# Performance work log

Hardware: AMD Instinct MI355X
Metric: run time of the kernel (lower is better)

The kernel has to match this reference:

```python
import jax, jax.numpy as jnp
from jax import lax
import numpy as np

B, T, F = 4, 2048, 128
DM, L, STRIDE, KF = 512, 4, 4, 2
N, DC, E = 16, 4, 2
DI = E * DM          # 1024 inner dim
R = (DM + 15) // 16  # 32 dt_rank
K = KF * STRIDE      # 8 front conv kernel
EPS = 1e-5

def _ln(x, w, b):
    m = x.mean(-1, keepdims=True)
    v = ((x - m) ** 2).mean(-1, keepdims=True)
    return (x - m) / jnp.sqrt(v + EPS) * w + b

def _causal_dwconv(x, w, b):
    # x: (B,Ts,DI), w: (DI,DC) depthwise causal conv
    xc = x.transpose(0, 2, 1)
    y = lax.conv_general_dilated(xc, w[:, None, :], (1,), [(DC - 1, 0)],
                                 feature_group_count=w.shape[0])
    return (y + b[None, :, None]).transpose(0, 2, 1)

def _selective_scan(dt, A, Bm, Cm, u):
    # dt,u: (B,Ts,DI); A: (DI,N); Bm,Cm: (B,Ts,N)
    dA = jnp.exp(dt[..., None] * A)                  # (B,Ts,DI,N)
    dBu = (dt * u)[..., None] * Bm[:, :, None, :]    # (B,Ts,DI,N)
    def step(h, inp):
        dA_t, dBu_t, C_t = inp
        h = dA_t * h + dBu_t
        y = jnp.einsum('bdn,bn->bd', h, C_t)
        return h, y
    h0 = jnp.zeros((u.shape[0], DI, N), u.dtype)
    _, ys = lax.scan(step, h0, (dA.transpose(1, 0, 2, 3),
                                dBu.transpose(1, 0, 2, 3),
                                Cm.transpose(1, 0, 2)))
    return ys.transpose(1, 0, 2)

def _mamba(x, in_w, cw, cb, xp_w, dtp_w, dtp_b, A_log, Dp, out_w):
    xz = jnp.einsum('btd,ed->bte', x, in_w)          # (B,Ts,2*DI)
    xi, z = jnp.split(xz, 2, axis=-1)
    xi = jax.nn.silu(_causal_dwconv(xi, cw, cb))
    x_dbl = jnp.einsum('btd,ed->bte', xi, xp_w)      # (B,Ts,R+2N)
    dt, Bm, Cm = jnp.split(x_dbl, [R, R + N], axis=-1)
    dt = jax.nn.softplus(jnp.einsum('btr,dr->btd', dt, dtp_w) + dtp_b)
    y = _selective_scan(dt, -jnp.exp(A_log), Bm, Cm, xi)
    y = (y + xi * Dp) * jax.nn.silu(z)
    return jnp.einsum('btd,od->bto', y, out_w)

def _forward(x, conv_w, conv_b, in_proj_w, conv1d_w, conv1d_b, x_proj_w,
             dt_proj_w, dt_proj_b, A_log, D_skip, ln_w, ln_b, out_proj_w,
             norm_w, norm_b):
    T_orig = x.shape[1]
    # causal strided front conv: pad (K-1,0), stride=STRIDE, then GELU
    h = lax.conv_general_dilated(x.transpose(0, 2, 1), conv_w, (STRIDE,),
                                 [(K - 1, 0)])
    h = jax.nn.gelu((h + conv_b[None, :, None]).transpose(0, 2, 1),
                    approximate=False)               # (B,T//STRIDE,DM)
    for l in range(L):
        hn = _ln(h, ln_w[l], ln_b[l])
        h = h + _mamba(hn, in_proj_w[l], conv1d_w[l], conv1d_b[l],
                       x_proj_w[l], dt_proj_w[l], dt_proj_b[l],
                       A_log[l], D_skip[l], out_proj_w[l])
    h = _ln(h, norm_w, norm_b)
    # repeat_interleave upsample back to original resolution
    return jnp.repeat(h, STRIDE, axis=1)[:, :T_orig, :]

def setup_inputs():
    key = jax.random.key(0)
    ks = jax.random.split(key, 8)
    g = lambda i, shape, s=0.02: jax.random.normal(ks[i], shape, jnp.float32) * s
    A_log = jnp.tile(jnp.log(jnp.arange(1, N + 1, dtype=jnp.float32)), (L, DI, 1))
    return dict(
        x=jax.random.normal(ks[0], (B, T, F), jnp.float32),
        conv_w=g(1, (DM, F, K)), conv_b=jnp.zeros((DM,), jnp.float32),
        in_proj_w=g(2, (L, 2 * DI, DM)),
        conv1d_w=g(3, (L, DI, DC), 0.2),
        conv1d_b=jnp.zeros((L, DI), jnp.float32),
        x_proj_w=g(4, (L, R + 2 * N, DI)),
        dt_proj_w=g(5, (L, DI, R), 0.1),
        dt_proj_b=jnp.full((L, DI), -2.0, jnp.float32),
        A_log=A_log,
        D_skip=jnp.ones((L, DI), jnp.float32),
        ln_w=jnp.ones((L, DM), jnp.float32),
        ln_b=jnp.zeros((L, DM), jnp.float32),
        out_proj_w=g(6, (L, DM, DI)),
        norm_w=jnp.ones((DM,), jnp.float32),
        norm_b=jnp.zeros((DM,), jnp.float32),
    )

def reference(x, conv_w, conv_b, in_proj_w, conv1d_w, conv1d_b, x_proj_w,
              dt_proj_w, dt_proj_b, A_log, D_skip, ln_w, ln_b, out_proj_w,
              norm_w, norm_b):
    return _forward(x, conv_w, conv_b, in_proj_w, conv1d_w, conv1d_b, x_proj_w,
                    dt_proj_w, dt_proj_b, A_log, D_skip, ln_w, ln_b, out_proj_w,
                    norm_w, norm_b)
```

## Files before the change

kernel.cpp:

```cpp
#include <hip/hip_runtime.h>
#include <hip/hip_bf16.h>

typedef unsigned short u16;
typedef u16 u16x8 __attribute__((ext_vector_type(8)));
typedef __bf16 bf16x8 __attribute__((ext_vector_type(8)));
typedef float f32x4 __attribute__((ext_vector_type(4)));

#define GLOAD16(gsrc, ldst) \
  __builtin_amdgcn_global_load_lds((const __attribute__((address_space(1))) void*)(gsrc), \
                                   (__attribute__((address_space(3))) void*)(ldst), 16, 0, 0)

__device__ __forceinline__ u16 f2bf(float f) {
  union { float f; unsigned u; } c; c.f = f;
  unsigned r = c.u + 0x7FFFu + ((c.u >> 16) & 1u);
  return (u16)(r >> 16);
}
__device__ __forceinline__ float bf2f(u16 v) {
  union { unsigned u; float f; } c; c.u = ((unsigned)v) << 16;
  return c.f;
}

__global__ __launch_bounds__(256) void cast_weights_k(
    const float* __restrict__ in_w, const float* __restrict__ xp_w,
    const float* __restrict__ out_w, const float* __restrict__ conv_w,
    const float* __restrict__ A_log, const float* __restrict__ c1w,
    u16* __restrict__ winb, u16* __restrict__ wxpb, u16* __restrict__ woutb,
    u16* __restrict__ wconvb, float* __restrict__ Apre, float* __restrict__ cwt) {
  int i = blockIdx.x * 256 + threadIdx.x;
  if (i < 1048576) {
    const float4 v = *(const float4*)(in_w + (size_t)i * 4);
    ushort2 lo = {f2bf(v.x), f2bf(v.y)}, hi = {f2bf(v.z), f2bf(v.w)};
    *(ushort2*)(winb + (size_t)i * 4) = lo;
    *(ushort2*)(winb + (size_t)i * 4 + 2) = hi;
    return;
  }
  i -= 1048576;
  if (i < 65536) {
    const float4 v = *(const float4*)(xp_w + (size_t)i * 4);
    ushort2 lo = {f2bf(v.x), f2bf(v.y)}, hi = {f2bf(v.z), f2bf(v.w)};
    *(ushort2*)(wxpb + (size_t)i * 4) = lo;
    *(ushort2*)(wxpb + (size_t)i * 4 + 2) = hi;
    return;
  }
  i -= 65536;
  if (i < 524288) {
    const float4 v = *(const float4*)(out_w + (size_t)i * 4);
    ushort2 lo = {f2bf(v.x), f2bf(v.y)}, hi = {f2bf(v.z), f2bf(v.w)};
    *(ushort2*)(woutb + (size_t)i * 4) = lo;
    *(ushort2*)(woutb + (size_t)i * 4 + 2) = hi;
    return;
  }
  i -= 524288;
  if (i < 131072) {
    const int m = i >> 8, r = (i & 255) * 4;
    const int kk = r >> 7, ff = r & 127;
    const float* src = conv_w + m * 1024 + kk;
    ushort2 lo = {f2bf(src[(ff + 0) * 8]), f2bf(src[(ff + 1) * 8])};
    ushort2 hi = {f2bf(src[(ff + 2) * 8]), f2bf(src[(ff + 3) * 8])};
    *(ushort2*)(wconvb + (size_t)i * 4) = lo;
    *(ushort2*)(wconvb + (size_t)i * 4 + 2) = hi;
    return;
  }
  i -= 131072;
  if (i < 16384) {
    const float4 v = *(const float4*)(A_log + (size_t)i * 4);
    float4 o;
    o.x = -__expf(v.x); o.y = -__expf(v.y); o.z = -__expf(v.z); o.w = -__expf(v.w);
    *(float4*)(Apre + (size_t)i * 4) = o;
    return;
  }
  i -= 16384;
  if (i < 4096) {
    const int og = i * 4, l = og >> 12, r = og & 4095;
    const int j = r >> 10, d0 = r & 1023;
    float4 o;
    o.x = c1w[l * 4096 + (d0 + 0) * 4 + j];
    o.y = c1w[l * 4096 + (d0 + 1) * 4 + j];
    o.z = c1w[l * 4096 + (d0 + 2) * 4 + j];
    o.w = c1w[l * 4096 + (d0 + 3) * 4 + j];
    *(float4*)(cwt + (size_t)i * 4) = o;
  }
}

__global__ __launch_bounds__(256) void im2col_k(const float* __restrict__ x,
                                                u16* __restrict__ xc) {
  const int i = blockIdx.x * 256 + threadIdx.x;
  const int col = (i & 255) * 4, tok = i >> 8;
  const int kk = col >> 7, ff = col & 127;
  const int b = tok >> 9, to = tok & 511;
  const int t = to * 4 + kk - 7;
  float4 v = {0.f, 0.f, 0.f, 0.f};
  if (t >= 0) v = *(const float4*)(x + ((size_t)b * 2048 + t) * 128 + ff);
  ushort2 lo = {f2bf(v.x), f2bf(v.y)}, hi = {f2bf(v.z), f2bf(v.w)};
  *(ushort2*)(xc + (size_t)i * 4) = lo;
  *(ushort2*)(xc + (size_t)i * 4 + 2) = hi;
}

template <int NW>
__global__ __launch_bounds__(NW * 64) void gemm2_k(
    const u16* __restrict__ A, int lda, const u16* __restrict__ Bw, int ldb,
    u16* __restrict__ C, int ldc, int Ks, size_t mn) {
  __shared__ __align__(16) char smem[NW * 32768];
  const int tid = threadIdx.x, lane = tid & 63, wid = tid >> 6;
  const int bm = blockIdx.x, bn = blockIdx.y;
  const int Kw = Ks / NW;
  const size_t koff = (size_t)blockIdx.z * Ks + (size_t)wid * Kw;
  char* base = smem + wid * 32768;
  const int srow = lane >> 2, sslot = lane & 3;
  const int nk = Kw >> 5;
  f32x4 acc[4][4] = {};

  auto stage = [&](int buf, int kt) {
#pragma unroll
    for (int c = 0; c < 8; ++c) {
      int lrow, gr, ldx; const u16* src;
      if (c < 4) { lrow = c * 16 + srow; gr = bm * 64 + lrow; src = A; ldx = lda; }
      else { lrow = (c - 4) * 16 + srow; gr = bn * 64 + lrow; src = Bw; ldx = ldb; }
      const int slot = sslot ^ ((lrow >> 1) & 3);
      GLOAD16(src + (size_t)gr * ldx + koff + kt * 32 + slot * 8,
              base + buf * 8192 + c * 1024);
    }
  };

  stage(0, 0);
  if (nk > 1) stage(1, 1);
  if (nk > 2) stage(2, 2);
  const int s = lane >> 4, r0 = lane & 15;
  for (int kt = 0; kt < nk; ++kt) {
    const int p = kt & 3;
    if (kt + 2 < nk)      asm volatile("s_waitcnt vmcnt(16)" ::: "memory");
    else if (kt + 1 < nk) asm volatile("s_waitcnt vmcnt(8)" ::: "memory");
    else                  asm volatile("s_waitcnt vmcnt(0)" ::: "memory");
    __builtin_amdgcn_sched_barrier(0);
    bf16x8 af[4], bfv[4];
#pragma unroll
    for (int i = 0; i < 4; ++i) {
      const int r = i * 16 + r0;
      af[i] = *(const bf16x8*)(base + p * 8192 + r * 64 + ((s ^ ((r >> 1) & 3)) << 4));
      bfv[i] = *(const bf16x8*)(base + p * 8192 + 4096 + r * 64 + ((s ^ ((r >> 1) & 3)) << 4));
    }
#pragma unroll
    for (int mi = 0; mi < 4; ++mi)
#pragma unroll
      for (int ni = 0; ni < 4; ++ni)
        acc[mi][ni] = __builtin_amdgcn_mfma_f32_16x16x32_bf16(af[mi], bfv[ni],
                                                              acc[mi][ni], 0, 0, 0);
    __builtin_amdgcn_sched_barrier(0);
    if (kt + 3 < nk) stage((kt + 3) & 3, kt + 3);
  }
  if constexpr (NW == 2) {
    if (wid == 1) {
      f32x4* dst = (f32x4*)(smem + 32768);
#pragma unroll
      for (int mi = 0; mi < 4; ++mi)
#pragma unroll
        for (int ni = 0; ni < 4; ++ni)
          dst[(mi * 4 + ni) * 64 + lane] = acc[mi][ni];
    }
    __syncthreads();
    if (wid == 1) return;
    const f32x4* src1 = (const f32x4*)(smem + 32768);
#pragma unroll
    for (int mi = 0; mi < 4; ++mi)
#pragma unroll
      for (int ni = 0; ni < 4; ++ni)
        acc[mi][ni] += src1[(mi * 4 + ni) * 64 + lane];
  }
  const int er0 = lane & 15, eg4 = lane >> 4;
  u16* Cz = C + (size_t)blockIdx.z * mn;
#pragma unroll
  for (int mi = 0; mi < 4; ++mi)
#pragma unroll
    for (int ni = 0; ni < 4; ++ni) {
      const int col = bn * 64 + ni * 16 + er0;
#pragma unroll
      for (int r = 0; r < 4; ++r) {
        const int row = bm * 64 + mi * 16 + eg4 * 4 + r;
        Cz[(size_t)row * ldc + col] = f2bf(acc[mi][ni][r]);
      }
    }
}

template <int MODE>
__global__ __launch_bounds__(256) void red_ln_k(
    const u16* __restrict__ P, float* __restrict__ h,
    const float* __restrict__ bias, const float* __restrict__ w,
    const float* __restrict__ bb, u16* __restrict__ o, float* __restrict__ oup) {
  const int row = blockIdx.x * 4 + (threadIdx.x >> 6);
  const int lane = threadIdx.x & 63;
  const size_t base = (size_t)row * 512 + lane * 8;
  float v[8];
  if constexpr (MODE == 0) {
#pragma unroll
    for (int j = 0; j < 8; ++j) v[j] = 0.f;
  } else {
    float4 a = *(const float4*)(h + base);
    float4 b4 = *(const float4*)(h + base + 4);
    v[0] = a.x; v[1] = a.y; v[2] = a.z; v[3] = a.w;
    v[4] = b4.x; v[5] = b4.y; v[6] = b4.z; v[7] = b4.w;
  }
#pragma unroll
  for (int s2 = 0; s2 < 4; ++s2) {
    const u16x8 pv = *(const u16x8*)(P + (size_t)s2 * 1048576 + base);
#pragma unroll
    for (int j = 0; j < 8; ++j) v[j] += bf2f(pv[j]);
  }
  if constexpr (MODE == 0) {
    const int col = lane * 8;
#pragma unroll
    for (int j = 0; j < 8; ++j) {
      const float t = v[j] + bias[col + j];
      v[j] = 0.5f * t * (1.f + erff(t * 0.70710678118f));
    }
  }
  if constexpr (MODE != 2) {
    float4 oa; oa.x = v[0]; oa.y = v[1]; oa.z = v[2]; oa.w = v[3];
    float4 ob; ob.x = v[4]; ob.y = v[5]; ob.z = v[6]; ob.w = v[7];
    *(float4*)(h + base) = oa;
    *(float4*)(h + base + 4) = ob;
  }
  float s = 0.f, sq = 0.f;
#pragma unroll
  for (int j = 0; j < 8; ++j) { s += v[j]; sq += v[j] * v[j]; }
  for (int off = 32; off; off >>= 1) { s += __shfl_xor(s, off); sq += __shfl_xor(sq, off); }
  const float m = s * (1.f / 512.f);
  const float rs = rsqrtf(sq * (1.f / 512.f) - m * m + 1e-5f);
  const float* wp = w + lane * 8; const float* bp = bb + lane * 8;
  float nv[8];
#pragma unroll
  for (int j = 0; j < 8; ++j) nv[j] = (v[j] - m) * rs * wp[j] + bp[j];
  if constexpr (MODE != 2) {
    uint4 uu;
    uu.x = (unsigned)f2bf(nv[0]) | ((unsigned)f2bf(nv[1]) << 16);
    uu.y = (unsigned)f2bf(nv[2]) | ((unsigned)f2bf(nv[3]) << 16);
    uu.z = (unsigned)f2bf(nv[4]) | ((unsigned)f2bf(nv[5]) << 16);
    uu.w = (unsigned)f2bf(nv[6]) | ((unsigned)f2bf(nv[7]) << 16);
    *(uint4*)(o + base) = uu;
  } else {
    const int bi = row >> 9, t0 = row & 511;
    float4 lo; lo.x = nv[0]; lo.y = nv[1]; lo.z = nv[2]; lo.w = nv[3];
    float4 hi; hi.x = nv[4]; hi.y = nv[5]; hi.z = nv[6]; hi.w = nv[7];
    float* obp = oup + ((size_t)bi * 2048 + (size_t)t0 * 4) * 512 + lane * 8;
#pragma unroll
    for (int q = 0; q < 4; ++q) {
      *(float4*)(obp + (size_t)q * 512) = lo;
      *(float4*)(obp + (size_t)q * 512 + 4) = hi;
    }
  }
}

__global__ __launch_bounds__(256) void redx_k(const u16* __restrict__ P,
                                              float* __restrict__ C) {
  const size_t i8 = ((size_t)blockIdx.x * 256 + threadIdx.x) * 8;
  if (i8 >= 131072) return;
  float v[8] = {};
#pragma unroll
  for (int s2 = 0; s2 < 4; ++s2) {
    const u16x8 pv = *(const u16x8*)(P + (size_t)s2 * 131072 + i8);
#pragma unroll
    for (int j = 0; j < 8; ++j) v[j] += bf2f(pv[j]);
  }
  float4 a; a.x = v[0]; a.y = v[1]; a.z = v[2]; a.w = v[3];
  float4 b; b.x = v[4]; b.y = v[5]; b.z = v[6]; b.w = v[7];
  *(float4*)(C + i8) = a;
  *(float4*)(C + i8 + 4) = b;
}

__global__ __launch_bounds__(256) void dtproj_k(const float* __restrict__ xdbl,
                                                const float* __restrict__ dtw,
                                                const float* __restrict__ dtbias,
                                                u16* __restrict__ dtbb) {
  __shared__ float xls[32 * 32];
  const int tid = threadIdx.x;
  const int dc = (blockIdx.x & 3) * 256;
  const int tg = (blockIdx.x >> 2) * 32;
  const int d = dc + tid;
  float4 w[8];
#pragma unroll
  for (int j = 0; j < 8; ++j) w[j] = *(const float4*)(dtw + (size_t)d * 32 + j * 4);
  for (int i = tid; i < 1024; i += 256) {
    const int t = i >> 5, r = i & 31;
    xls[i] = xdbl[(size_t)(tg + t) * 64 + r];
  }
  const float b = dtbias[d];
  __syncthreads();
  for (int t = 0; t < 32; ++t) {
    const float4* xr = (const float4*)&xls[t * 32];
    float acc = b;
#pragma unroll
    for (int j = 0; j < 8; ++j) {
      const float4 xv = xr[j];
      acc = fmaf(w[j].x, xv.x, acc); acc = fmaf(w[j].y, xv.y, acc);
      acc = fmaf(w[j].z, xv.z, acc); acc = fmaf(w[j].w, xv.w, acc);
    }
    dtbb[(size_t)(tg + t) * 1024 + d] =
        f2bf(fmaxf(acc, 0.f) + __logf(1.f + __expf(-fabsf(acc))));
  }
}

__global__ __launch_bounds__(256) void dwconv_k(const u16* __restrict__ xzb,
                                                const float* __restrict__ cwt,
                                                const float* __restrict__ cb,
                                                u16* __restrict__ xib) {
  const int i = blockIdx.x * 256 + threadIdx.x;
  const int d0 = (i & 127) * 8, tok = i >> 7, t = tok & 511;
  const u16* p = xzb + (size_t)tok * 2048 + d0;
  const float4 b0 = *(const float4*)(cb + d0);
  const float4 b1 = *(const float4*)(cb + d0 + 4);
  float acc[8] = {b0.x, b0.y, b0.z, b0.w, b1.x, b1.y, b1.z, b1.w};
#pragma unroll
  for (int j = 0; j < 4; ++j) {
    const int ts = t + j - 3;
    if (ts >= 0) {
      const u16x8 xv = *(const u16x8*)(p + (j - 3) * 2048);
      const float4 wa = *(const float4*)(cwt + j * 1024 + d0);
      const float4 wb = *(const float4*)(cwt + j * 1024 + d0 + 4);
      acc[0] = fmaf(bf2f(xv[0]), wa.x, acc[0]);
      acc[1] = fmaf(bf2f(xv[1]), wa.y, acc[1]);
      acc[2] = fmaf(bf2f(xv[2]), wa.z, acc[2]);
      acc[3] = fmaf(bf2f(xv[3]), wa.w, acc[3]);
      acc[4] = fmaf(bf2f(xv[4]), wb.x, acc[4]);
      acc[5] = fmaf(bf2f(xv[5]), wb.y, acc[5]);
      acc[6] = fmaf(bf2f(xv[6]), wb.z, acc[6]);
      acc[7] = fmaf(bf2f(xv[7]), wb.w, acc[7]);
    }
  }
  u16x8 o;
#pragma unroll
  for (int e = 0; e < 8; ++e)
    o[e] = f2bf(acc[e] / (1.f + __expf(-acc[e])));
  *(u16x8*)(xib + (size_t)i * 8) = o;
}

__global__ __launch_bounds__(256) void scan1_k(const u16* __restrict__ dtbb,
                                               const u16* __restrict__ xib,
                                               const float* __restrict__ xd,
                                               const float* __restrict__ Ap,
                                               float* __restrict__ hF,
                                               float* __restrict__ aP) {
  const int blk = blockIdx.x;
  const int d = (blk & 3) * 256 + threadIdx.x;
  const int c = (blk >> 2) & 31, b = blk >> 7;
  float A[16], h[16], ap[16];
#pragma unroll
  for (int n = 0; n < 16; ++n) { A[n] = Ap[d * 16 + n]; h[n] = 0.f; ap[n] = 1.f; }
  const int t0 = c * 16;
  for (int t = t0; t < t0 + 16; ++t) {
    const int tok = b * 512 + t;
    const float dtv = bf2f(dtbb[(size_t)tok * 1024 + d]);
    const float u = bf2f(xib[(size_t)tok * 1024 + d]);
    const float s = dtv * u;
    const float* Bp = xd + (size_t)tok * 64 + 32;
#pragma unroll
    for (int n = 0; n < 16; ++n) {
      const float dA = __expf(dtv * A[n]);
      h[n] = dA * h[n] + s * Bp[n];
      ap[n] *= dA;
    }
  }
#pragma unroll
  for (int n = 0; n < 16; ++n) {
    const size_t o = ((size_t)(b * 32 + c) * 16 + n) * 1024 + d;
    hF[o] = h[n]; aP[o] = ap[n];
  }
}

__global__ __launch_bounds__(256) void scan2_k(const float* __restrict__ hF,
                                               const float* __restrict__ aP,
                                               float* __restrict__ hI) {
  const int bi = blockIdx.x >> 6;
  const int n = (blockIdx.x >> 2) & 15;
  const int d = (blockIdx.x & 3) * 256 + threadIdx.x;
  float h = 0.f;
  for (int c = 0; c < 32; ++c) {
    const size_t o = ((size_t)((bi * 32 + c) * 16 + n)) * 1024 + d;
    hI[o] = h;
    h = fmaf(aP[o], h, hF[o]);
  }
}

__global__ __launch_bounds__(256) void scan3_k(const u16* __restrict__ dtbb,
                                               const u16* __restrict__ xib,
                                               const float* __restrict__ xd,
                                               const float* __restrict__ Ap,
                                               const float* __restrict__ hI,
                                               const u16* __restrict__ xzb,
                                               const float* __restrict__ Dp,
                                               u16* __restrict__ y2b) {
  const int blk = blockIdx.x;
  const int d = (blk & 3) * 256 + threadIdx.x;
  const int c = (blk >> 2) & 31, b = blk >> 7;
  float A[16], h[16];
#pragma unroll
  for (int n = 0; n < 16; ++n) {
    A[n] = Ap[d * 16 + n];
    h[n] = hI[((size_t)(b * 32 + c) * 16 + n) * 1024 + d];
  }
  const float Dd = Dp[d];
  const int t0 = c * 16;
  for (int t = t0; t < t0 + 16; ++t) {
    const int tok = b * 512 + t;
    const float dtv = bf2f(dtbb[(size_t)tok * 1024 + d]);
    const float u = bf2f(xib[(size_t)tok * 1024 + d]);
    const float s = dtv * u;
    const float* Bp = xd + (size_t)tok * 64 + 32;
    const float* Cp = xd + (size_t)tok * 64 + 48;
    float y = 0.f;
#pragma unroll
    for (int n = 0; n < 16; ++n) {
      const float dA = __expf(dtv * A[n]);
      h[n] = dA * h[n] + s * Bp[n];
      y = fmaf(h[n], Cp[n], y);
    }
    const float z = bf2f(xzb[(size_t)tok * 2048 + 1024 + d]);
    const float sz = z / (1.f + __expf(-z));
    y2b[(size_t)tok * 1024 + d] = f2bf((y + u * Dd) * sz);
  }
}

extern "C" void kernel_launch(void* const* d_in, const int* in_sizes, int n_in,
                              void* d_out, int out_size, void* d_ws, size_t ws_size,
                              hipStream_t stream) {
  const float* x      = (const float*)d_in[0];
  const float* conv_w = (const float*)d_in[1];
  const float* conv_b = (const float*)d_in[2];
  const float* in_w   = (const float*)d_in[3];
  const float* c1w    = (const float*)d_in[4];
  const float* c1b    = (const float*)d_in[5];
  const float* xp_w   = (const float*)d_in[6];
  const float* dt_w   = (const float*)d_in[7];
  const float* dt_b   = (const float*)d_in[8];
  const float* A_log  = (const float*)d_in[9];
  const float* D_skip = (const float*)d_in[10];
  const float* ln_w   = (const float*)d_in[11];
  const float* ln_b   = (const float*)d_in[12];
  const float* out_w  = (const float*)d_in[13];
  const float* norm_w = (const float*)d_in[14];
  const float* norm_b = (const float*)d_in[15];
  float* out = (float*)d_out;

  float* f = (float*)d_ws;
  float* h    = f; f += 1048576;
  float* xdbl = f; f += 131072;
  float* Apre = f; f += 65536;
  float* cwt  = f; f += 16384;
  float* hF   = f; f += 2097152;
  float* aP   = f; f += 2097152;
  float* hI   = f; f += 2097152;
  u16* ub = (u16*)f;
  u16* hnb    = ub; ub += 1048576;
  u16* xzb    = ub; ub += 4194304;
  u16* xib    = ub; ub += 2097152;
  u16* dtbb   = ub; ub += 2097152;
  u16* y2b    = ub; ub += 2097152;
  u16* xcolb  = ub; ub += 2097152;
  u16* pp     = ub; ub += 4194304;
  u16* ppB    = ub; ub += 524288;
  u16* winb   = ub; ub += 4194304;
  u16* wxpb   = ub; ub += 262144;
  u16* woutb  = ub; ub += 2097152;
  u16* wconvb = ub; ub += 524288;

  cast_weights_k<<<6993, 256, 0, stream>>>(in_w, xp_w, out_w, conv_w, A_log, c1w,
                                           winb, wxpb, woutb, wconvb, Apre, cwt);
  im2col_k<<<2048, 256, 0, stream>>>(x, xcolb);
  gemm2_k<2><<<dim3(32, 8, 4), 128, 0, stream>>>(xcolb, 1024, wconvb, 1024,
                                                 pp, 512, 256, (size_t)1048576);
  red_ln_k<0><<<512, 256, 0, stream>>>(pp, h, conv_b, ln_w, ln_b, hnb, nullptr);
  for (int l = 0; l < 4; ++l) {
    gemm2_k<2><<<dim3(32, 32, 1), 128, 0, stream>>>(hnb, 512, winb + l * 1048576,
                                                    512, xzb, 2048, 512, 0);
    dwconv_k<<<1024, 256, 0, stream>>>(xzb, cwt + l * 4096, c1b + l * 1024, xib);
    gemm2_k<2><<<dim3(32, 1, 4), 128, 0, stream>>>(xib, 1024, wxpb + l * 65536,
                                                   1024, ppB, 64, 256, (size_t)131072);
    redx_k<<<64, 256, 0, stream>>>(ppB, xdbl);
    dtproj_k<<<256, 256, 0, stream>>>(xdbl, dt_w + l * 32768, dt_b + l * 1024, dtbb);
    scan1_k<<<512, 256, 0, stream>>>(dtbb, xib, xdbl, Apre + l * 16384, hF, aP);
    scan2_k<<<256, 256, 0, stream>>>(hF, aP, hI);
    scan3_k<<<512, 256, 0, stream>>>(dtbb, xib, xdbl, Apre + l * 16384, hI, xzb,
                                     D_skip + l * 1024, y2b);
    gemm2_k<2><<<dim3(32, 8, 4), 128, 0, stream>>>(y2b, 1024, woutb + l * 524288,
                                                   1024, pp, 512, 256, (size_t)1048576);
    if (l < 3) {
      red_ln_k<1><<<512, 256, 0, stream>>>(pp, h, nullptr, ln_w + (l + 1) * 512,
                                           ln_b + (l + 1) * 512, hnb, nullptr);
    } else {
      red_ln_k<2><<<512, 256, 0, stream>>>(pp, h, nullptr, norm_w, norm_b,
                                           nullptr, out);
    }
  }
}
```

Baseline: 364.0 us.

## Fuse split-K reduction and dt projection into chunked scan kernels

Removes the separate x_proj split-K reduction kernel and the dt projection/softplus kernel. Both scan passes now reduce the four bf16 partials into shared memory and recompute dt per token in registers, so the bf16 dt buffer and the fp32 x_dbl buffer are no longer written or read. The scan chunk length doubles from 16 to 32 tokens, halving the chunk-state buffers and the scan2 work, but the scan kernels now launch 256 blocks instead of 512. This lowers parallelism, and the dt projection and partial reduction are done twice, once in each scan pass.

Result: slower. 387.4 us (+6.4%).

```diff
diff --git a/kernel.cpp b/kernel.cpp
--- a/kernel.cpp
+++ b/kernel.cpp
@@ -246,55 +246,6 @@
       *(float4*)(obp + (size_t)q * 512) = lo;
       *(float4*)(obp + (size_t)q * 512 + 4) = hi;
     }
-  }
-}
-
-__global__ __launch_bounds__(256) void redx_k(const u16* __restrict__ P,
-                                              float* __restrict__ C) {
-  const size_t i8 = ((size_t)blockIdx.x * 256 + threadIdx.x) * 8;
-  if (i8 >= 131072) return;
-  float v[8] = {};
-#pragma unroll
-  for (int s2 = 0; s2 < 4; ++s2) {
-    const u16x8 pv = *(const u16x8*)(P + (size_t)s2 * 131072 + i8);
-#pragma unroll
-    for (int j = 0; j < 8; ++j) v[j] += bf2f(pv[j]);
-  }
-  float4 a; a.x = v[0]; a.y = v[1]; a.z = v[2]; a.w = v[3];
-  float4 b; b.x = v[4]; b.y = v[5]; b.z = v[6]; b.w = v[7];
-  *(float4*)(C + i8) = a;
-  *(float4*)(C + i8 + 4) = b;
-}
-
-__global__ __launch_bounds__(256) void dtproj_k(const float* __restrict__ xdbl,
-                                                const float* __restrict__ dtw,
-                                                const float* __restrict__ dtbias,
-                                                u16* __restrict__ dtbb) {
-  __shared__ float xls[32 * 32];
-  const int tid = threadIdx.x;
-  const int dc = (blockIdx.x & 3) * 256;
-  const int tg = (blockIdx.x >> 2) * 32;
-  const int d = dc + tid;
-  float4 w[8];
-#pragma unroll
-  for (int j = 0; j < 8; ++j) w[j] = *(const float4*)(dtw + (size_t)d * 32 + j * 4);
-  for (int i = tid; i < 1024; i += 256) {
-    const int t = i >> 5, r = i & 31;
-    xls[i] = xdbl[(size_t)(tg + t) * 64 + r];
-  }
-  const float b = dtbias[d];
-  __syncthreads();
-  for (int t = 0; t < 32; ++t) {
-    const float4* xr = (const float4*)&xls[t * 32];
-    float acc = b;
-#pragma unroll
-    for (int j = 0; j < 8; ++j) {
-      const float4 xv = xr[j];
-      acc = fmaf(w[j].x, xv.x, acc); acc = fmaf(w[j].y, xv.y, acc);
-      acc = fmaf(w[j].z, xv.z, acc); acc = fmaf(w[j].w, xv.w, acc);
-    }
-    dtbb[(size_t)(tg + t) * 1024 + d] =
-        f2bf(fmaxf(acc, 0.f) + __logf(1.f + __expf(-fabsf(acc))));
   }
 }
 
@@ -332,35 +283,51 @@
   *(u16x8*)(xib + (size_t)i * 8) = o;
 }
 
-__global__ __launch_bounds__(256) void scan1_k(const u16* __restrict__ dtbb,
-                                               const u16* __restrict__ xib,
-                                               const float* __restrict__ xd,
-                                               const float* __restrict__ Ap,
-                                               float* __restrict__ hF,
-                                               float* __restrict__ aP) {
+__global__ __launch_bounds__(256) void scan1f_k(
+    const u16* __restrict__ ppB, const float* __restrict__ dtw,
+    const float* __restrict__ dtbias, const u16* __restrict__ xib,
+    const float* __restrict__ Ap, float* __restrict__ hF, float* __restrict__ aP) {
+  __shared__ float xls[32 * 64];
   const int blk = blockIdx.x;
-  const int d = (blk & 3) * 256 + threadIdx.x;
-  const int c = (blk >> 2) & 31, b = blk >> 7;
+  const int tid = threadIdx.x;
+  const int d = (blk & 3) * 256 + tid;
+  const int c = (blk >> 2) & 15, b = blk >> 6;
+  const int T0 = b * 512 + c * 32;
+  for (int i = tid; i < 2048; i += 256) {
+    const size_t off = (size_t)(T0 + (i >> 6)) * 64 + (i & 63);
+    xls[i] = bf2f(ppB[off]) + bf2f(ppB[131072 + off]) +
+             bf2f(ppB[262144 + off]) + bf2f(ppB[393216 + off]);
+  }
+  float4 w[8];
+#pragma unroll
+  for (int j = 0; j < 8; ++j) w[j] = *(const float4*)(dtw + (size_t)d * 32 + j * 4);
+  const float bia = dtbias[d];
   float A[16], h[16], ap[16];
 #pragma unroll
   for (int n = 0; n < 16; ++n) { A[n] = Ap[d * 16 + n]; h[n] = 0.f; ap[n] = 1.f; }
-  const int t0 = c * 16;
-  for (int t = t0; t < t0 + 16; ++t) {
-    const int tok = b * 512 + t;
-    const float dtv = bf2f(dtbb[(size_t)tok * 1024 + d]);
-    const float u = bf2f(xib[(size_t)tok * 1024 + d]);
-    const float s = dtv * u;
-    const float* Bp = xd + (size_t)tok * 64 + 32;
+  __syncthreads();
+  for (int t = 0; t < 32; ++t) {
+    const float* xr = &xls[t * 64];
+    float acc = bia;
+#pragma unroll
+    for (int j = 0; j < 8; ++j) {
+      const float4 xv = ((const float4*)xr)[j];
+      acc = fmaf(w[j].x, xv.x, acc); acc = fmaf(w[j].y, xv.y, acc);
+      acc = fmaf(w[j].z, xv.z, acc); acc = fmaf(w[j].w, xv.w, acc);
+    }
+    const float dt = fmaxf(acc, 0.f) + __logf(1.f + __expf(-fabsf(acc)));
+    const float u = bf2f(xib[(size_t)(T0 + t) * 1024 + d]);
+    const float s = dt * u;
 #pragma unroll
     for (int n = 0; n < 16; ++n) {
-      const float dA = __expf(dtv * A[n]);
-      h[n] = dA * h[n] + s * Bp[n];
+      const float dA = __expf(dt * A[n]);
+      h[n] = dA * h[n] + s * xr[32 + n];
       ap[n] *= dA;
     }
   }
 #pragma unroll
   for (int n = 0; n < 16; ++n) {
-    const size_t o = ((size_t)(b * 32 + c) * 16 + n) * 1024 + d;
+    const size_t o = ((size_t)(b * 16 + c) * 16 + n) * 1024 + d;
     hF[o] = h[n]; aP[o] = ap[n];
   }
 }
@@ -372,45 +339,61 @@
   const int n = (blockIdx.x >> 2) & 15;
   const int d = (blockIdx.x & 3) * 256 + threadIdx.x;
   float h = 0.f;
-  for (int c = 0; c < 32; ++c) {
-    const size_t o = ((size_t)((bi * 32 + c) * 16 + n)) * 1024 + d;
+  for (int c = 0; c < 16; ++c) {
+    const size_t o = ((size_t)((bi * 16 + c) * 16 + n)) * 1024 + d;
     hI[o] = h;
     h = fmaf(aP[o], h, hF[o]);
   }
 }
 
-__global__ __launch_bounds__(256) void scan3_k(const u16* __restrict__ dtbb,
-                                               const u16* __restrict__ xib,
-                                               const float* __restrict__ xd,
-                                               const float* __restrict__ Ap,
-                                               const float* __restrict__ hI,
-                                               const u16* __restrict__ xzb,
-                                               const float* __restrict__ Dp,
-                                               u16* __restrict__ y2b) {
+__global__ __launch_bounds__(256) void scan3f_k(
+    const u16* __restrict__ ppB, const float* __restrict__ dtw,
+    const float* __restrict__ dtbias, const u16* __restrict__ xib,
+    const float* __restrict__ Ap, const float* __restrict__ hI,
+    const u16* __restrict__ xzb, const float* __restrict__ Dp,
+    u16* __restrict__ y2b) {
+  __shared__ float xls[32 * 64];
   const int blk = blockIdx.x;
-  const int d = (blk & 3) * 256 + threadIdx.x;
-  const int c = (blk >> 2) & 31, b = blk >> 7;
+  const int tid = threadIdx.x;
+  const int d = (blk & 3) * 256 + tid;
+  const int c = (blk >> 2) & 15, b = blk >> 6;
+  const int T0 = b * 512 + c * 32;
+  for (int i = tid; i < 2048; i += 256) {
+    const size_t off = (size_t)(T0 + (i >> 6)) * 64 + (i & 63);
+    xls[i] = bf2f(ppB[off]) + bf2f(ppB[131072 + off]) +
+             bf2f(ppB[262144 + off]) + bf2f(ppB[393216 + off]);
+  }
+  float4 w[8];
+#pragma unroll
+  for (int j = 0; j < 8; ++j) w[j] = *(const float4*)(dtw + (size_t)d * 32 + j * 4);
+  const float bia = dtbias[d];
   float A[16], h[16];
 #pragma unroll
   for (int n = 0; n < 16; ++n) {
     A[n] = Ap[d * 16 + n];
-    h[n] = hI[((size_t)(b * 32 + c) * 16 + n) * 1024 + d];
+    h[n] = hI[((size_t)(b * 16 + c) * 16 + n) * 1024 + d];
   }
   const float Dd = Dp[d];
-  const int t0 = c * 16;
-  for (int t = t0; t < t0 + 16; ++t) {
-    const int tok = b * 512 + t;
-    const float dtv = bf2f(dtbb[(size_t)tok * 1024 + d]);
+  __syncthreads();
+  for (int t = 0; t < 32; ++t) {
+    const float* xr = &xls[t * 64];
+    float acc = bia;
+#pragma unroll
+    for (int j = 0; j < 8; ++j) {
+      const float4 xv = ((const float4*)xr)[j];
+      acc = fmaf(w[j].x, xv.x, acc); acc = fmaf(w[j].y, xv.y, acc);
+      acc = fmaf(w[j].z, xv.z, acc); acc = fmaf(w[j].w, xv.w, acc);
+    }
+    const float dt = fmaxf(acc, 0.f) + __logf(1.f + __expf(-fabsf(acc)));
+    const int tok = T0 + t;
     const float u = bf2f(xib[(size_t)tok * 1024 + d]);
-    const float s = dtv * u;
-    const float* Bp = xd + (size_t)tok * 64 + 32;
-    const float* Cp = xd + (size_t)tok * 64 + 48;
+    const float s = dt * u;
     float y = 0.f;
 #pragma unroll
     for (int n = 0; n < 16; ++n) {
-      const float dA = __expf(dtv * A[n]);
-      h[n] = dA * h[n] + s * Bp[n];
-      y = fmaf(h[n], Cp[n], y);
+      const float dA = __expf(dt * A[n]);
+      h[n] = dA * h[n] + s * xr[32 + n];
+      y = fmaf(h[n], xr[48 + n], y);
     }
     const float z = bf2f(xzb[(size_t)tok * 2048 + 1024 + d]);
     const float sz = z / (1.f + __expf(-z));
@@ -441,17 +424,15 @@
 
   float* f = (float*)d_ws;
   float* h    = f; f += 1048576;
-  float* xdbl = f; f += 131072;
   float* Apre = f; f += 65536;
   float* cwt  = f; f += 16384;
-  float* hF   = f; f += 2097152;
-  float* aP   = f; f += 2097152;
-  float* hI   = f; f += 2097152;
+  float* hF   = f; f += 1048576;
+  float* aP   = f; f += 1048576;
+  float* hI   = f; f += 1048576;
   u16* ub = (u16*)f;
   u16* hnb    = ub; ub += 1048576;
   u16* xzb    = ub; ub += 4194304;
   u16* xib    = ub; ub += 2097152;
-  u16* dtbb   = ub; ub += 2097152;
   u16* y2b    = ub; ub += 2097152;
   u16* xcolb  = ub; ub += 2097152;
   u16* pp     = ub; ub += 4194304;
@@ -473,12 +454,12 @@
     dwconv_k<<<1024, 256, 0, stream>>>(xzb, cwt + l * 4096, c1b + l * 1024, xib);
     gemm2_k<2><<<dim3(32, 1, 4), 128, 0, stream>>>(xib, 1024, wxpb + l * 65536,
                                                    1024, ppB, 64, 256, (size_t)131072);
-    redx_k<<<64, 256, 0, stream>>>(ppB, xdbl);
-    dtproj_k<<<256, 256, 0, stream>>>(xdbl, dt_w + l * 32768, dt_b + l * 1024, dtbb);
-    scan1_k<<<512, 256, 0, stream>>>(dtbb, xib, xdbl, Apre + l * 16384, hF, aP);
+    scan1f_k<<<256, 256, 0, stream>>>(ppB, dt_w + l * 32768, dt_b + l * 1024,
+                                      xib, Apre + l * 16384, hF, aP);
     scan2_k<<<256, 256, 0, stream>>>(hF, aP, hI);
-    scan3_k<<<512, 256, 0, stream>>>(dtbb, xib, xdbl, Apre + l * 16384, hI, xzb,
-                                     D_skip + l * 1024, y2b);
+    scan3f_k<<<256, 256, 0, stream>>>(ppB, dt_w + l * 32768, dt_b + l * 1024,
+                                      xib, Apre + l * 16384, hI, xzb,
+                                      D_skip + l * 1024, y2b);
     gemm2_k<2><<<dim3(32, 8, 4), 128, 0, stream>>>(y2b, 1024, woutb + l * 524288,
                                                    1024, pp, 512, 256, (size_t)1048576);
     if (l < 3) {
```
